# Performance work log

Measured on AMD Instinct MI355X. Metric: run time of the kernel, lower is better.

The kernel has to match this reference:

```python
import jax, jax.numpy as jnp
import numpy as np

N_EMBED = 384

def setup_inputs() -> dict:
    key = jax.random.key(0)
    kx, kq, kk, kv = jax.random.split(key, 4)
    B, T, C = 512, 256, N_EMBED
    H = 64
    scale = 1.0 / np.sqrt(C)  # param init scale, keep activations sane
    x = jax.random.normal(kx, (B, T, C), dtype=jnp.float32)
    Wq = jax.random.normal(kq, (C, H), dtype=jnp.float32) * scale
    Wk = jax.random.normal(kk, (C, H), dtype=jnp.float32) * scale
    Wv = jax.random.normal(kv, (C, H), dtype=jnp.float32) * scale
    return {"x": x, "Wq": Wq, "Wk": Wk, "Wv": Wv}

def reference(x, Wq, Wk, Wv):
    B, T, C = x.shape
    q = jnp.einsum('btc,ch->bth', x, Wq)
    k = jnp.einsum('btc,ch->bth', x, Wk)
    v = jnp.einsum('btc,ch->bth', x, Wv)
    # NOTE: original scales by C**-0.5 with C = n_embed (384), not head_size.
    wei = jnp.einsum('bth,bsh->bts', q, k) * (C ** -0.5)  # [B,T,T]
    causal = jnp.tril(jnp.ones((T, T), dtype=bool))
    wei = jnp.where(causal, wei, -jnp.inf)
    wei = jax.nn.softmax(wei, axis=-1)
    out = jnp.einsum('bts,bsh->bth', wei, v)  # [B,T,H]
    return out
```

## Files before the change

kernel.cpp:

```cpp
#include <hip/hip_runtime.h>
#include <hip/hip_bf16.h>


constexpr int BSZ  = 512;
constexpr int TT   = 256;
constexpr int CDIM = 384;
constexpr int HDIM = 64;
constexpr int NQKV = 192;
constexpr float SCALE2 = 0.07362222313880647f;
constexpr int BTST = 392;

typedef __attribute__((ext_vector_type(8))) short bf16x8;
typedef __attribute__((ext_vector_type(4))) float f32x4;

__device__ inline unsigned short f2bf(float f) {
    __hip_bfloat16 h = __float2bfloat16(f);
    return *(unsigned short*)&h;
}
__device__ inline bf16x8 pack8(float4 a, float4 b) {
    unsigned short p[8] = { f2bf(a.x), f2bf(a.y), f2bf(a.z), f2bf(a.w),
                            f2bf(b.x), f2bf(b.y), f2bf(b.z), f2bf(b.w) };
    return *(bf16x8*)p;
}
__device__ inline unsigned cvtpk(float lo, float hi) {
    unsigned r;
    asm volatile("v_cvt_pk_bf16_f32 %0, %1, %2" : "=v"(r) : "v"(lo), "v"(hi));
    return r;
}
#define PLSWAP32(a, b) asm volatile("v_permlane32_swap_b32 %0, %1" : "+v"(a), "+v"(b))
#define PLSWAP16(a, b) asm volatile("v_permlane16_swap_b32 %0, %1" : "+v"(a), "+v"(b))

__global__ __launch_bounds__(256) void prep_bt(
    const float* __restrict__ Wq, const float* __restrict__ Wk,
    const float* __restrict__ Wv, unsigned short* __restrict__ bt)
{
    int idx = blockIdx.x * 256 + threadIdx.x;
    if (idx >= NQKV * CDIM) return;
    int n = idx / CDIM, k = idx - n * CDIM;
    const float* W = (n < 64) ? Wq : (n < 128) ? Wk : Wv;
    bt[idx] = f2bf(W[(size_t)k * HDIM + (n & 63)]);
}

__global__ __launch_bounds__(1024) void fused(
    const float* __restrict__ x, const unsigned short* __restrict__ bt,
    float* __restrict__ out)
{
    __shared__ __align__(16) unsigned short smem[NQKV * BTST];
    unsigned short* btl = smem;
    unsigned short* qs  = smem;
    unsigned short* kl  = smem + 16384;
    unsigned short* vt  = smem + 32768;

    const int b = blockIdx.x, tid = threadIdx.x;
    const int w = tid >> 6, lane = tid & 63;
    const int lr = lane & 15, lk = lane >> 4;

    const float* xr0 = x + ((size_t)b * TT + 16 * w + lr) * CDIM + lk * 8;

    float4 pA[2], pB[2], pC[2];
#define LDCH(P, ks) { \
    P[0] = *(const float4*)&xr0[(ks) * 32];     \
    P[1] = *(const float4*)&xr0[(ks) * 32 + 4]; }
#define STEP(P, ks, cond) { \
    bf16x8 a = pack8(P[0], P[1]); \
    if (cond) LDCH(P, (ks) + 3); \
    _Pragma("unroll") \
    for (int ni = 0; ni < 12; ++ni) { \
        bf16x8 bb = *(const bf16x8*)&btl[(ni * 16 + lr) * BTST + (ks) * 32 + lk * 8]; \
        acc[ni] = __builtin_amdgcn_mfma_f32_16x16x32_bf16(a, bb, acc[ni], 0, 0, 0); \
    } }

    LDCH(pA, 0) LDCH(pB, 1) LDCH(pC, 2)

    #pragma unroll
    for (int p = 0; p < 9; ++p) {
        int i = p * 1024 + tid;
        int row = i / 48, c8 = i - row * 48;
        *(uint4*)&btl[row * BTST + c8 * 8] = ((const uint4*)bt)[i];
    }
    __syncthreads();

    f32x4 acc[12];
    #pragma unroll
    for (int ni = 0; ni < 12; ++ni) acc[ni] = (f32x4){0.f, 0.f, 0.f, 0.f};

    #pragma unroll
    for (int kk = 0; kk < 4; ++kk) {
        STEP(pA, 3 * kk + 0, kk < 3)
        STEP(pB, 3 * kk + 1, kk < 3)
        STEP(pC, 3 * kk + 2, kk < 3)
    }
#undef LDCH
#undef STEP
    __syncthreads();

    unsigned short* pq = qs + w * 1024;
    #pragma unroll
    for (int ni = 0; ni < 4; ++ni)
        #pragma unroll
        for (int r = 0; r < 4; ++r) {
            int qr = lk * 4 + r;
            int h  = ni * 16 + lr;
            pq[qr * 64 + (h ^ ((qr & 7) << 3))] = f2bf(acc[ni][r] * SCALE2);
        }
    #pragma unroll
    for (int ni = 4; ni < 8; ++ni)
        #pragma unroll
        for (int r = 0; r < 4; ++r) {
            int row = 16 * w + lk * 4 + r;
            int c2  = (ni - 4) * 16 + lr;
            kl[row * 64 + (c2 ^ ((row & 7) << 3))] = f2bf(acc[ni][r]);
        }
    #pragma unroll
    for (int ni = 8; ni < 12; ++ni) {
        int h  = (ni - 8) * 16 + lr;
        int t0 = 16 * w + lk * 4;
        unsigned short pk[4];
        #pragma unroll
        for (int r = 0; r < 4; ++r) pk[r] = f2bf(acc[ni][r]);
        *(uint2*)&vt[h * 256 + (t0 ^ ((h & 7) << 3))] = *(uint2*)pk;
    }
    __syncthreads();

    const int q0 = 16 * w;
    bf16x8 qa[2];
    #pragma unroll
    for (int kc = 0; kc < 2; ++kc)
        qa[kc] = *(const bf16x8*)&pq[lr * 64 + ((kc * 32 + lk * 8) ^ ((lr & 7) << 3))];

    f32x4 oacc[4];
    float mrowL = -INFINITY;
    float lpart = 0.f;
    #pragma unroll
    for (int nh = 0; nh < 4; ++nh) oacc[nh] = (f32x4){0.f, 0.f, 0.f, 0.f};

    const int lastt = w >> 2;
    for (int st = 0; st <= lastt; ++st) {
        f32x4 sa[4];
        #pragma unroll
        for (int ni = 0; ni < 4; ++ni) sa[ni] = (f32x4){0.f, 0.f, 0.f, 0.f};
        #pragma unroll
        for (int ni = 0; ni < 4; ++ni) {
            int row = st * 64 + ni * 16 + lr;
            #pragma unroll
            for (int kc = 0; kc < 2; ++kc) {
                bf16x8 kb = *(const bf16x8*)
                    &kl[row * 64 + ((kc * 32 + lk * 8) ^ ((row & 7) << 3))];
                sa[ni] = __builtin_amdgcn_mfma_f32_16x16x32_bf16(kb, qa[kc], sa[ni], 0, 0, 0);
            }
        }
        if (st == lastt) {
            #pragma unroll
            for (int ni = 0; ni < 4; ++ni) {
                #pragma unroll
                for (int r = 0; r < 4; ++r) {
                    int sg = st * 64 + ni * 16 + lk * 4 + r;
                    if (sg > q0 + lr) sa[ni][r] = -INFINITY;
                }
            }
        }
        float pm = sa[0][0];
        #pragma unroll
        for (int ni = 0; ni < 4; ++ni)
            #pragma unroll
            for (int r = 0; r < 4; ++r) pm = fmaxf(pm, sa[ni][r]);
        pm = fmaxf(pm, __shfl_xor(pm, 16));
        pm = fmaxf(pm, __shfl_xor(pm, 32));
        if (!__all(pm - mrowL <= 8.0f)) {
            float mn = fmaxf(mrowL, pm);
            float corr = exp2f(mrowL - mn);
            mrowL = mn;
            lpart *= corr;
            #pragma unroll
            for (int r = 0; r < 4; ++r) {
                float ct = __shfl(corr, lk * 4 + r);
                #pragma unroll
                for (int nh = 0; nh < 4; ++nh) oacc[nh][r] *= ct;
            }
        }
        #pragma unroll
        for (int ni = 0; ni < 4; ++ni)
            #pragma unroll
            for (int r = 0; r < 4; ++r) {
                float p = exp2f(sa[ni][r] - mrowL);
                sa[ni][r] = p;
                lpart += p;
            }
        unsigned Wp[4][2];
        #pragma unroll
        for (int ni = 0; ni < 4; ++ni) {
            Wp[ni][0] = cvtpk(sa[ni][0], sa[ni][1]);
            Wp[ni][1] = cvtpk(sa[ni][2], sa[ni][3]);
        }
        bf16x8 pa[2];
        #pragma unroll
        for (int kc = 0; kc < 2; ++kc) {
            unsigned x0 = Wp[2 * kc][0], y0 = Wp[2 * kc + 1][0];
            PLSWAP32(x0, y0); PLSWAP16(x0, y0);
            unsigned x1 = Wp[2 * kc][1], y1 = Wp[2 * kc + 1][1];
            PLSWAP32(x1, y1); PLSWAP16(x1, y1);
            unsigned wq[4] = {x0, x1, y0, y1};
            pa[kc] = *(bf16x8*)wq;
        }
        #pragma unroll
        for (int nh = 0; nh < 4; ++nh) {
            int hrow = nh * 16 + lr;
            #pragma unroll
            for (int kc = 0; kc < 2; ++kc) {
                bf16x8 vb = *(const bf16x8*)
                    &vt[hrow * 256 + ((st * 64 + kc * 32 + lk * 8) ^ ((hrow & 7) << 3))];
                oacc[nh] = __builtin_amdgcn_mfma_f32_16x16x32_bf16(pa[kc], vb, oacc[nh], 0, 0, 0);
            }
        }
    }

    float lsum = lpart;
    lsum += __shfl_xor(lsum, 16);
    lsum += __shfl_xor(lsum, 32);
    float linv[4];
    #pragma unroll
    for (int r = 0; r < 4; ++r)
        linv[r] = 1.0f / __shfl(lsum, lk * 4 + r);
    #pragma unroll
    for (int nh = 0; nh < 4; ++nh)
        #pragma unroll
        for (int r = 0; r < 4; ++r) {
            size_t row = (size_t)b * TT + q0 + lk * 4 + r;
            out[row * HDIM + nh * 16 + lr] = oacc[nh][r] * linv[r];
        }
}

extern "C" void kernel_launch(void* const* d_in, const int* in_sizes, int n_in,
                              void* d_out, int out_size, void* d_ws, size_t ws_size,
                              hipStream_t stream)
{
    const float* x  = (const float*)d_in[0];
    const float* Wq = (const float*)d_in[1];
    const float* Wk = (const float*)d_in[2];
    const float* Wv = (const float*)d_in[3];
    unsigned short* bt = (unsigned short*)d_ws;
    float* out = (float*)d_out;

    prep_bt<<<(NQKV * CDIM + 255) / 256, 256, 0, stream>>>(Wq, Wk, Wv, bt);
    fused<<<BSZ, 1024, 0, stream>>>(x, bt, out);
}
```

Baseline: 62.94 us.

## Use 32x32x16 MFMA tiles for QKV projection with 2D wave partition

Reworks the QKV projection stage: each wave now computes a 32-row by 96-column block with three 32x32x16 bf16 MFMAs per k-step, instead of a 16-row by 192-column block with twelve 16x16x32 MFMAs. This cuts LDS reads of the weight tile per wave (each B fragment is reused across 32 rows) and uses the larger MFMA shape. The epilogue scatter into Q/K/V shared buffers is rewritten for the 32x32 accumulator layout, and Q is read from a shared layout indexed by global row. Risks include more k-steps and register-prefetch iterations, and divergent branches in the epilogue.

```diff
diff --git a/kernel.cpp b/kernel.cpp
--- a/kernel.cpp
+++ b/kernel.cpp
@@ -12,6 +12,7 @@
 
 typedef __attribute__((ext_vector_type(8))) short bf16x8;
 typedef __attribute__((ext_vector_type(4))) float f32x4;
+typedef __attribute__((ext_vector_type(16))) float f32x16;
 
 __device__ inline unsigned short f2bf(float f) {
     __hip_bfloat16 h = __float2bfloat16(f);
@@ -54,20 +55,23 @@
     const int b = blockIdx.x, tid = threadIdx.x;
     const int w = tid >> 6, lane = tid & 63;
     const int lr = lane & 15, lk = lane >> 4;
-
-    const float* xr0 = x + ((size_t)b * TT + 16 * w + lr) * CDIM + lk * 8;
+    const int l31 = lane & 31, l5 = lane >> 5;
+
+    const int mg = w >> 1, ng = w & 1;
+    const float* xr = x + ((size_t)b * TT + 32 * mg + l31) * CDIM + l5 * 8;
 
     float4 pA[2], pB[2], pC[2];
 #define LDCH(P, ks) { \
-    P[0] = *(const float4*)&xr0[(ks) * 32];     \
-    P[1] = *(const float4*)&xr0[(ks) * 32 + 4]; }
+    P[0] = *(const float4*)&xr[(ks) * 16];     \
+    P[1] = *(const float4*)&xr[(ks) * 16 + 4]; }
 #define STEP(P, ks, cond) { \
     bf16x8 a = pack8(P[0], P[1]); \
     if (cond) LDCH(P, (ks) + 3); \
     _Pragma("unroll") \
-    for (int ni = 0; ni < 12; ++ni) { \
-        bf16x8 bb = *(const bf16x8*)&btl[(ni * 16 + lr) * BTST + (ks) * 32 + lk * 8]; \
-        acc[ni] = __builtin_amdgcn_mfma_f32_16x16x32_bf16(a, bb, acc[ni], 0, 0, 0); \
+    for (int ci = 0; ci < 3; ++ci) { \
+        bf16x8 bb = *(const bf16x8*) \
+            &btl[(96 * ng + 32 * ci + l31) * BTST + (ks) * 16 + l5 * 8]; \
+        acc[ci] = __builtin_amdgcn_mfma_f32_32x32x16_bf16(a, bb, acc[ci], 0, 0, 0); \
     } }
 
     LDCH(pA, 0) LDCH(pB, 1) LDCH(pC, 2)
@@ -80,45 +84,54 @@
     }
     __syncthreads();
 
-    f32x4 acc[12];
-    #pragma unroll
-    for (int ni = 0; ni < 12; ++ni) acc[ni] = (f32x4){0.f, 0.f, 0.f, 0.f};
-
-    #pragma unroll
-    for (int kk = 0; kk < 4; ++kk) {
-        STEP(pA, 3 * kk + 0, kk < 3)
-        STEP(pB, 3 * kk + 1, kk < 3)
-        STEP(pC, 3 * kk + 2, kk < 3)
+    f32x16 acc[3];
+    #pragma unroll
+    for (int ci = 0; ci < 3; ++ci)
+        #pragma unroll
+        for (int r = 0; r < 16; ++r) acc[ci][r] = 0.f;
+
+    #pragma unroll
+    for (int kk = 0; kk < 8; ++kk) {
+        STEP(pA, 3 * kk + 0, kk < 7)
+        STEP(pB, 3 * kk + 1, kk < 7)
+        STEP(pC, 3 * kk + 2, kk < 7)
     }
 #undef LDCH
 #undef STEP
     __syncthreads();
 
-    unsigned short* pq = qs + w * 1024;
-    #pragma unroll
-    for (int ni = 0; ni < 4; ++ni)
-        #pragma unroll
-        for (int r = 0; r < 4; ++r) {
-            int qr = lk * 4 + r;
-            int h  = ni * 16 + lr;
-            pq[qr * 64 + (h ^ ((qr & 7) << 3))] = f2bf(acc[ni][r] * SCALE2);
-        }
-    #pragma unroll
-    for (int ni = 4; ni < 8; ++ni)
-        #pragma unroll
-        for (int r = 0; r < 4; ++r) {
-            int row = 16 * w + lk * 4 + r;
-            int c2  = (ni - 4) * 16 + lr;
-            kl[row * 64 + (c2 ^ ((row & 7) << 3))] = f2bf(acc[ni][r]);
-        }
-    #pragma unroll
-    for (int ni = 8; ni < 12; ++ni) {
-        int h  = (ni - 8) * 16 + lr;
-        int t0 = 16 * w + lk * 4;
-        unsigned short pk[4];
-        #pragma unroll
-        for (int r = 0; r < 4; ++r) pk[r] = f2bf(acc[ni][r]);
-        *(uint2*)&vt[h * 256 + (t0 ^ ((h & 7) << 3))] = *(uint2*)pk;
+    #pragma unroll
+    for (int ci = 0; ci < 3; ++ci) {
+        const int col = 96 * ng + 32 * ci + l31;
+        if (col < 64) {
+            #pragma unroll
+            for (int g = 0; g < 4; ++g)
+                #pragma unroll
+                for (int r = 0; r < 4; ++r) {
+                    int row = 32 * mg + r + 8 * g + 4 * l5;
+                    qs[row * 64 + (col ^ ((row & 7) << 3))] =
+                        f2bf(acc[ci][4 * g + r] * SCALE2);
+                }
+        } else if (col < 128) {
+            int c2 = col - 64;
+            #pragma unroll
+            for (int g = 0; g < 4; ++g)
+                #pragma unroll
+                for (int r = 0; r < 4; ++r) {
+                    int row = 32 * mg + r + 8 * g + 4 * l5;
+                    kl[row * 64 + (c2 ^ ((row & 7) << 3))] = f2bf(acc[ci][4 * g + r]);
+                }
+        } else {
+            int h = col - 128;
+            #pragma unroll
+            for (int g = 0; g < 4; ++g) {
+                int t0 = 32 * mg + 8 * g + 4 * l5;
+                unsigned short pk[4];
+                #pragma unroll
+                for (int r = 0; r < 4; ++r) pk[r] = f2bf(acc[ci][4 * g + r]);
+                *(uint2*)&vt[h * 256 + (t0 ^ ((h & 7) << 3))] = *(uint2*)pk;
+            }
+        }
     }
     __syncthreads();
 
@@ -126,7 +139,8 @@
     bf16x8 qa[2];
     #pragma unroll
     for (int kc = 0; kc < 2; ++kc)
-        qa[kc] = *(const bf16x8*)&pq[lr * 64 + ((kc * 32 + lk * 8) ^ ((lr & 7) << 3))];
+        qa[kc] = *(const bf16x8*)
+            &qs[(q0 + lr) * 64 + ((kc * 32 + lk * 8) ^ ((lr & 7) << 3))];
 
     f32x4 oacc[4];
     float mrowL = -INFINITY;
@@ -151,13 +165,12 @@
         }
         if (st == lastt) {
             #pragma unroll
-            for (int ni = 0; ni < 4; ++ni) {
+            for (int ni = 0; ni < 4; ++ni)
                 #pragma unroll
                 for (int r = 0; r < 4; ++r) {
                     int sg = st * 64 + ni * 16 + lk * 4 + r;
                     if (sg > q0 + lr) sa[ni][r] = -INFINITY;
                 }
-            }
         }
         float pm = sa[0][0];
         #pragma unroll
```

After: 76.37 us. 1.21x slower.
